# Kernel optimization log

Measured on AMD Instinct MI355X. Metric: run time of the kernel, lower is better.

## Reference

```python
import jax, jax.numpy as jnp
import numpy as np

RATIO = 1.0 / 32  # spacial_ratio
HOUT = 7          # pooled_h
WOUT = 7          # pooled_w
S = 2             # sub_bin_size = int(sqrt(n_sampled=4))


def setup_inputs() -> dict:
    key = jax.random.key(0)
    k1, k2, k3, k4, k5, k6 = jax.random.split(key, 6)
    B, C, H, W = 4, 256, 50, 50
    N = 1024
    img_w, img_h = W / RATIO, H / RATIO
    features = jax.random.normal(k1, (B, C, H, W), dtype=jnp.float32)
    b = jax.random.randint(k2, (N,), 0, B).astype(jnp.float32)
    x1 = jax.random.uniform(k3, (N,), minval=0.0, maxval=img_w - 232.0)
    y1 = jax.random.uniform(k4, (N,), minval=0.0, maxval=img_h - 232.0)
    bw = jax.random.uniform(k5, (N,), minval=32.0, maxval=232.0)
    bh = jax.random.uniform(k6, (N,), minval=32.0, maxval=232.0)
    rois = jnp.stack([b, x1, y1, x1 + bw, y1 + bh], axis=1)  # [N, 5]
    return {"features": features, "rois": rois}


def _roi_align(features, rois):
    B, C, H, W = features.shape
    fW = jnp.float32(W)
    fH = jnp.float32(H)
    b_idx = rois[:, 0].astype(jnp.int32)            # [N]
    box = rois[:, 1:] * RATIO                       # [N, 4] in feature coords
    bx1 = jnp.clip(box[:, 0], 0.0, fW)
    by1 = jnp.clip(box[:, 1], 0.0, fH)
    bx2 = jnp.clip(box[:, 2], 0.0, fW)
    by2 = jnp.clip(box[:, 3], 0.0, fH)
    roi_valid = (bx2 - bx1 > 0) & (by2 - by1 > 0)   # [N]
    bin_w = (bx2 - bx1) / WOUT                      # [N]
    bin_h = (by2 - by1) / HOUT

    jj = jnp.arange(WOUT, dtype=jnp.float32)
    ii = jnp.arange(HOUT, dtype=jnp.float32)
    # bin edges; y2/x2 computed from the UNclamped start, then clamped (matches original order)
    x1u = bx1[:, None] + jj * bin_w[:, None]        # [N, WOUT]
    x2b = jnp.clip(x1u + bin_w[:, None], 0.0, fW)
    x1b = jnp.clip(x1u, 0.0, fW)
    y1u = by1[:, None] + ii * bin_h[:, None]        # [N, HOUT]
    y2b = jnp.clip(y1u + bin_h[:, None], 0.0, fH)
    y1b = jnp.clip(y1u, 0.0, fH)
    bin_valid = (y2b > y1b)[:, :, None] & (x2b > x1b)[:, None, :]  # [N, HOUT, WOUT]

    # SxS sample-point centers inside each bin (sub_bin = bin / S, center offset 0.5)
    cc = jnp.arange(S, dtype=jnp.float32) + 0.5
    px = x1b[:, :, None] + cc * (bin_w / S)[:, None, None]  # [N, WOUT, S]
    py = y1b[:, :, None] + cc * (bin_h / S)[:, None, None]  # [N, HOUT, S]

    xl = jnp.clip(jnp.floor(px), 0, W - 1).astype(jnp.int32)
    xh = jnp.clip(xl + 1, 0, W - 1)
    yl = jnp.clip(jnp.floor(py), 0, H - 1).astype(jnp.int32)
    yh = jnp.clip(yl + 1, 0, H - 1)
    wxh = px - xl  # (x - x1)
    wxl = xh - px  # (x2 - x)
    wyb = py - yl  # (y - y1)
    wyt = yh - py  # (y2 - y)

    feats = features.transpose(0, 2, 3, 1)          # [B, H, W, C]
    bI = b_idx[:, None, None, None, None]           # [N,1,1,1,1]
    # x varies over (WOUT, sx) -> broadcast axes (2,4); y over (HOUT, sy) -> axes (1,3)
    XL = xl[:, None, :, None, :]
    XH = xh[:, None, :, None, :]
    YL = yl[:, :, None, :, None]
    YH = yh[:, :, None, :, None]
    WXh = wxh[:, None, :, None, :, None]
    WXl = wxl[:, None, :, None, :, None]
    WYb = wyb[:, :, None, :, None, None]
    WYt = wyt[:, :, None, :, None, None]

    v_tl = feats[bI, YL, XL]   # [N, HOUT, WOUT, S, S, C]
    v_tr = feats[bI, YL, XH]
    v_bl = feats[bI, YH, XL]
    v_br = feats[bI, YH, XH]
    top = WXh * v_tr + WXl * v_tl
    bot = WXh * v_br + WXl * v_bl
    val = WYb * bot + WYt * top                     # [N, HOUT, WOUT, S, S, C]

    pooled = val.max(axis=(3, 4))                   # max over sample grid -> [N, HOUT, WOUT, C]
    mask = bin_valid & roi_valid[:, None, None]
    pooled = jnp.where(mask[..., None], pooled, 0.0)
    return pooled.transpose(0, 3, 1, 2)             # [N, C, HOUT, WOUT]


def reference(features, rois):
    return _roi_align(features, rois)
```

## Files before the change

kernel.cpp:

```cpp
#include <hip/hip_runtime.h>


namespace {

constexpr int B_ = 4, C_ = 256, H_ = 50, W_ = 50;
constexpr int HW = H_ * W_;
constexpr int HO = 7, WO = 7, NBIN = HO * WO;
constexpr int OUT_PER_ROI = C_ * NBIN;
constexpr int LD = 260;
constexpr float RATIO = 1.0f / 32.0f;

__global__ __launch_bounds__(256) void transpose_tiled(
    const float* __restrict__ f, float* __restrict__ ft)
{
    __shared__ float tile[64][65];
    const int bt   = blockIdx.x;
    const int hw_t = bt % 40;
    const int c_t  = (bt / 40) % 4;
    const int b    = bt / 160;
    const int hw0 = hw_t * 64, c0 = c_t * 64;
    const int lx = threadIdx.x & 63;
    const int ly = threadIdx.x >> 6;

#pragma unroll
    for (int k = 0; k < 16; ++k) {
        const int c  = c0 + k * 4 + ly;
        const int hw = hw0 + lx;
        if (hw < HW)
            tile[k * 4 + ly][lx] = f[((size_t)b * C_ + c) * HW + hw];
    }
    __syncthreads();
#pragma unroll
    for (int k = 0; k < 16; ++k) {
        const int hw = hw0 + k * 4 + ly;
        if (hw < HW)
            ft[((size_t)b * HW + hw) * C_ + c0 + lx] = tile[lx][k * 4 + ly];
    }
}

__global__ __launch_bounds__(256) void roialign_main(
    const float* __restrict__ ft,
    const float* __restrict__ rois,
    float* __restrict__ out)
{
    __shared__ float stage[NBIN * LD];
    __shared__ __align__(16) float  wts[NBIN][8];
    __shared__ __align__(16) unsigned int offs[NBIN][8];

    const int n    = blockIdx.x;
    const int tid  = threadIdx.x;
    const int wave = tid >> 6;
    const int lane = tid & 63;
    const float fW = (float)W_, fH = (float)H_;

    if (tid < NBIN) {
        const int ii = tid / WO, jj = tid % WO;
        const float* r = rois + n * 5;
        const float bx1 = fminf(fmaxf(r[1] * RATIO, 0.0f), fW);
        const float by1 = fminf(fmaxf(r[2] * RATIO, 0.0f), fH);
        const float bx2 = fminf(fmaxf(r[3] * RATIO, 0.0f), fW);
        const float by2 = fminf(fmaxf(r[4] * RATIO, 0.0f), fH);
        const bool roi_valid = (bx2 - bx1 > 0.0f) && (by2 - by1 > 0.0f);
        const float bin_w = (bx2 - bx1) * (1.0f / (float)WO);
        const float bin_h = (by2 - by1) * (1.0f / (float)HO);

        const float x1u = bx1 + (float)jj * bin_w;
        const float x1b = fminf(fmaxf(x1u, 0.0f), fW);
        const float x2b = fminf(fmaxf(x1u + bin_w, 0.0f), fW);
        const float y1u = by1 + (float)ii * bin_h;
        const float y1b = fminf(fmaxf(y1u, 0.0f), fH);
        const float y2b = fminf(fmaxf(y1u + bin_h, 0.0f), fH);
        const float vf = (roi_valid && (y2b > y1b) && (x2b > x1b)) ? 1.0f : 0.0f;

        int xl[2], xh[2], yl[2], yh[2];
#pragma unroll
        for (int s = 0; s < 2; ++s) {
            const float px = x1b + ((float)s + 0.5f) * (bin_w * 0.5f);
            int l = (int)floorf(px);
            l = min(max(l, 0), W_ - 1);
            const int h = min(l + 1, W_ - 1);
            xl[s] = l; xh[s] = h;
            wts[tid][0 + s] = vf * (px - (float)l);
            wts[tid][2 + s] = vf * ((float)h - px);

            const float py = y1b + ((float)s + 0.5f) * (bin_h * 0.5f);
            int t = (int)floorf(py);
            t = min(max(t, 0), H_ - 1);
            const int u = min(t + 1, H_ - 1);
            yl[s] = t; yh[s] = u;
            wts[tid][4 + s] = py - (float)t;
            wts[tid][6 + s] = (float)u - py;
        }
#pragma unroll
        for (int sy = 0; sy < 2; ++sy) {
#pragma unroll
            for (int sx = 0; sx < 2; ++sx) {
                const int s = sy * 2 + sx;
                const unsigned tl = (unsigned)(yl[sy] * W_ + xl[sx]);
                const unsigned tr = (unsigned)(yl[sy] * W_ + xh[sx]);
                const unsigned bl = (unsigned)(yh[sy] * W_ + xl[sx]);
                const unsigned br = (unsigned)(yh[sy] * W_ + xh[sx]);
                offs[tid][s * 2 + 0] = tl | (tr << 16);
                offs[tid][s * 2 + 1] = bl | (br << 16);
            }
        }
    }
    __syncthreads();

    int b = (int)rois[n * 5];
    b = min(max(b, 0), B_ - 1);
    const float4* pb = (const float4*)(ft + (size_t)b * HW * C_) + lane;

    for (int bin = wave; bin < NBIN; bin += 4) {
        const float4 wa = *(const float4*)wts[bin];
        const float4 wb = *(const float4*)(wts[bin] + 4);
        const uint4  oa = *(const uint4*)offs[bin];
        const uint4  ob = *(const uint4*)(offs[bin] + 4);

        auto samp = [&](unsigned ptop, unsigned pbot,
                        float wxh, float wxl, float wyb, float wyt) -> float4 {
            const int tl = (int)(ptop & 0xffffu) << 6;
            const int tr = (int)(ptop >> 16) << 6;
            const int bl = (int)(pbot & 0xffffu) << 6;
            const int br = (int)(pbot >> 16) << 6;
            const float4 v_tl = pb[tl], v_tr = pb[tr];
            const float4 v_bl = pb[bl], v_br = pb[br];
            float4 o;
            o.x = wyb * (wxh * v_br.x + wxl * v_bl.x) + wyt * (wxh * v_tr.x + wxl * v_tl.x);
            o.y = wyb * (wxh * v_br.y + wxl * v_bl.y) + wyt * (wxh * v_tr.y + wxl * v_tl.y);
            o.z = wyb * (wxh * v_br.z + wxl * v_bl.z) + wyt * (wxh * v_tr.z + wxl * v_tl.z);
            o.w = wyb * (wxh * v_br.w + wxl * v_bl.w) + wyt * (wxh * v_tr.w + wxl * v_tl.w);
            return o;
        };

        const float4 s0 = samp(oa.x, oa.y, wa.x, wa.z, wb.x, wb.z);
        const float4 s1 = samp(oa.z, oa.w, wa.y, wa.w, wb.x, wb.z);
        const float4 s2 = samp(ob.x, ob.y, wa.x, wa.z, wb.y, wb.w);
        const float4 s3 = samp(ob.z, ob.w, wa.y, wa.w, wb.y, wb.w);
        float4 m;
        m.x = fmaxf(fmaxf(s0.x, s1.x), fmaxf(s2.x, s3.x));
        m.y = fmaxf(fmaxf(s0.y, s1.y), fmaxf(s2.y, s3.y));
        m.z = fmaxf(fmaxf(s0.z, s1.z), fmaxf(s2.z, s3.z));
        m.w = fmaxf(fmaxf(s0.w, s1.w), fmaxf(s2.w, s3.w));

        *(float4*)&stage[bin * LD + 4 * lane] = m;
    }
    __syncthreads();

    float* outn = out + (size_t)n * OUT_PER_ROI;
    for (int k = tid; k < OUT_PER_ROI; k += 256) {
        const int ch  = k / NBIN;
        const int bin = k - ch * NBIN;
        outn[k] = stage[bin * LD + ch];
    }
}

}

extern "C" void kernel_launch(void* const* d_in, const int* in_sizes, int n_in,
                              void* d_out, int out_size, void* d_ws, size_t ws_size,
                              hipStream_t stream)
{
    const float* feats = (const float*)d_in[0];
    const float* rois  = (const float*)d_in[1];
    float* out = (float*)d_out;
    const int N = in_sizes[1] / 5;
    float* ft = (float*)d_ws;

    hipLaunchKernelGGL(transpose_tiled, dim3(B_ * 4 * 40), dim3(256), 0, stream,
                       feats, ft);
    hipLaunchKernelGGL(roialign_main, dim3(N), dim3(256), 0, stream,
                       ft, rois, out);
}
```

Before: 107.1 us.

## Split ROI channels across two blocks to shrink shared staging and raise occupancy

The main kernel now launches two blocks per ROI, each handling 128 of the 256 channels, so the shared staging buffer is roughly halved. Each wave processes two bins at once, with half-waves of 32 lanes, and clamps the bin index at the tail. A launch-bounds minimum of 5 blocks per CU is added to push occupancy up. The trade-off is that the per-ROI bin setup (weights and offsets) is computed twice, and the gather loads are narrower per half-wave.

```diff
diff --git a/kernel.cpp b/kernel.cpp
--- a/kernel.cpp
+++ b/kernel.cpp
@@ -7,7 +7,9 @@
 constexpr int HW = H_ * W_;
 constexpr int HO = 7, WO = 7, NBIN = HO * WO;
 constexpr int OUT_PER_ROI = C_ * NBIN;
-constexpr int LD = 260;
+constexpr int CPB = 128;
+constexpr int COLS = CPB / 4;
+constexpr int LDs = 132;
 constexpr float RATIO = 1.0f / 32.0f;
 
 __global__ __launch_bounds__(256) void transpose_tiled(
@@ -38,19 +40,22 @@
     }
 }
 
-__global__ __launch_bounds__(256) void roialign_main(
+__global__ __launch_bounds__(256, 5) void roialign_main(
     const float* __restrict__ ft,
     const float* __restrict__ rois,
     float* __restrict__ out)
 {
-    __shared__ float stage[NBIN * LD];
-    __shared__ __align__(16) float  wts[NBIN][8];
-    __shared__ __align__(16) unsigned int offs[NBIN][8];
+    __shared__ float stage[NBIN * LDs];
+    __shared__ __align__(16) float    wts[NBIN][8];
+    __shared__ __align__(16) unsigned offs[NBIN][8];
 
     const int n    = blockIdx.x;
+    const int half = blockIdx.y;
     const int tid  = threadIdx.x;
     const int wave = tid >> 6;
     const int lane = tid & 63;
+    const int col  = lane & 31;
+    const int sub  = lane >> 5;
     const float fW = (float)W_, fH = (float)H_;
 
     if (tid < NBIN) {
@@ -109,13 +114,15 @@
 
     int b = (int)rois[n * 5];
     b = min(max(b, 0), B_ - 1);
-    const float4* pb = (const float4*)(ft + (size_t)b * HW * C_) + lane;
+    const float4* pb = (const float4*)(ft + (size_t)b * HW * C_) + half * COLS + col;
 
-    for (int bin = wave; bin < NBIN; bin += 4) {
-        const float4 wa = *(const float4*)wts[bin];
-        const float4 wb = *(const float4*)(wts[bin] + 4);
-        const uint4  oa = *(const uint4*)offs[bin];
-        const uint4  ob = *(const uint4*)(offs[bin] + 4);
+    for (int i0 = wave * 2; i0 < NBIN; i0 += 8) {
+        const int bin = i0 + sub;
+        const int bc  = min(bin, NBIN - 1);
+        const float4 wa = *(const float4*)wts[bc];
+        const float4 wb = *(const float4*)(wts[bc] + 4);
+        const uint4  oa = *(const uint4*)&offs[bc][0];
+        const uint4  ob = *(const uint4*)&offs[bc][4];
 
         auto samp = [&](unsigned ptop, unsigned pbot,
                         float wxh, float wxl, float wyb, float wyt) -> float4 {
@@ -143,15 +150,16 @@
         m.z = fmaxf(fmaxf(s0.z, s1.z), fmaxf(s2.z, s3.z));
         m.w = fmaxf(fmaxf(s0.w, s1.w), fmaxf(s2.w, s3.w));
 
-        *(float4*)&stage[bin * LD + 4 * lane] = m;
+        if (bin < NBIN)
+            *(float4*)&stage[bin * LDs + 4 * col] = m;
     }
     __syncthreads();
 
-    float* outn = out + (size_t)n * OUT_PER_ROI;
-    for (int k = tid; k < OUT_PER_ROI; k += 256) {
-        const int ch  = k / NBIN;
-        const int bin = k - ch * NBIN;
-        outn[k] = stage[bin * LD + ch];
+    float* outn = out + (size_t)n * OUT_PER_ROI + half * (CPB * NBIN);
+    for (int k = tid; k < CPB * NBIN; k += 256) {
+        const int ch = k / NBIN;
+        const int bi = k - ch * NBIN;
+        outn[k] = stage[bi * LDs + ch];
     }
 }
 
@@ -169,6 +177,6 @@
 
     hipLaunchKernelGGL(transpose_tiled, dim3(B_ * 4 * 40), dim3(256), 0, stream,
                        feats, ft);
-    hipLaunchKernelGGL(roialign_main, dim3(N), dim3(256), 0, stream,
+    hipLaunchKernelGGL(roialign_main, dim3(N, 2), dim3(256), 0, stream,
                        ft, rois, out);
 }
```

After: 105.0 us. 1.02x faster.
